# Kernel tuning notes

Hardware: AMD Instinct MI355X
Metric: run time of the kernel (lower is better)

The kernel has to match this reference:

```python
import math
import jax, jax.numpy as jnp
import numpy as np

B, T, D, K, R, KC = 4, 2048, 1024, 8, 16, 4
H = 4 * D  # mlp hidden


def setup_inputs() -> dict:
    key = jax.random.key(0)
    ks = jax.random.split(key, 12)
    s = lambda i, shape: jax.random.normal(ks[i], shape, jnp.float32) * 0.02
    # state_decay_logit init: geometric decays in [dmin, dmax], logit = log(p) - log1p(-p)
    dmin, dmax = 0.9, 0.999
    dec = np.exp(np.linspace(math.log(dmin), math.log(dmax), K))
    decay_logit = jnp.asarray(np.log(dec) - np.log1p(-dec), jnp.float32)
    return dict(
        x=jax.random.normal(ks[0], (B, T, D), jnp.float32),
        conv_w=s(1, (D, 1, KC)),            # depthwise conv kernel (torch Conv1d weight)
        gp_w=s(2, (D, D)), gp_b=jnp.zeros((D,), jnp.float32),
        up_w=s(3, (D, H)), up_b=jnp.zeros((H,), jnp.float32),
        dn_w=s(4, (H, D)), dn_b=jnp.zeros((D,), jnp.float32),
        si_w=s(5, (D, K * D)),              # state_in (no bias)
        so_w=s(6, (K * D, D)),              # state_out (no bias)
        decay_logit=decay_logit,
        rs_w=s(7, (D, R)), rs_b=jnp.zeros((R,), jnp.float32),
        rwg_w=s(8, (D, 1)), rwg_b=jnp.zeros((1,), jnp.float32),
        rv_w=s(9, (D, D)), rv_b=jnp.zeros((D,), jnp.float32),
        gr_w=s(10, (D, 1)), gr_b=jnp.zeros((1,), jnp.float32),
        gl_w=s(11, (D, 1)), gl_b=jnp.zeros((1,), jnp.float32),
    )


def _rms_norm(x, eps=1e-6):
    return x * jax.lax.rsqrt(jnp.mean(x * x, axis=-1, keepdims=True) + eps)


def _forward(x, conv_w, gp_w, gp_b, up_w, up_b, dn_w, dn_b, si_w, so_w,
             decay_logit, rs_w, rs_b, rwg_w, rwg_b, rv_w, rv_b, gr_w, gr_b, gl_w, gl_b):
    Bx, Tx, Dx = x.shape
    u = _rms_norm(x)
    # --- local mixer: causal depthwise conv + sigmoid gate + SiLU MLP ---
    xc = jax.lax.conv_general_dilated(
        jnp.swapaxes(u, 1, 2), conv_w, window_strides=(1,),
        padding=[(KC - 1, 0)], feature_group_count=Dx,
        dimension_numbers=('NCH', 'OIH', 'NCH'))
    xc = jnp.swapaxes(xc, 1, 2)                       # (B,T,D) causal conv output
    xg = xc * jax.nn.sigmoid(xc @ gp_w + gp_b)
    local = jax.nn.silu(xg @ up_w + up_b) @ dn_w + dn_b
    # --- per-channel exponential-decay state + register read/write scan ---
    dec = jax.nn.sigmoid(decay_logit)                 # (K,)
    z = (u @ si_w).reshape(Bx, Tx, K, Dx)             # state_in, (B,T,K,D)
    sel = jax.nn.softmax(u @ rs_w + rs_b, axis=-1)    # soft register address (B,T,R)
    wg = jax.nn.sigmoid(u @ rwg_w + rwg_b)            # write gate (B,T,1)
    v = u @ rv_w + rv_b                                # register value (B,T,D)

    def step(carry, inp):
        s, regs = carry
        z_t, sel_t, w_t, v_t = inp
        read = jnp.einsum('br,brd->bd', sel_t, regs)  # soft read before write
        ws = (w_t * sel_t)[:, :, None]                # (B,R,1)
        regs = regs * (1.0 - ws) + ws * v_t[:, None, :]
        s = dec[None, :, None] * s + z_t
        return (s, regs), (s, read)

    init = (jnp.zeros((Bx, K, Dx), x.dtype), jnp.zeros((Bx, R, Dx), x.dtype))
    tm = lambda a: jnp.swapaxes(a, 0, 1)              # time-major for scan
    _, (s_all, reads) = jax.lax.scan(step, init, (tm(z), tm(sel), tm(wg), tm(v)))
    s_all = tm(s_all)                                 # (B,T,K,D)
    reads = tm(reads)                                 # (B,T,D)
    long_out = jnp.einsum('btkd,kde->bte', s_all, so_w.reshape(K, Dx, Dx))
    g_long = jax.nn.sigmoid(u @ gl_w + gl_b)
    g_reg = jax.nn.sigmoid(u @ gr_w + gr_b)
    return x + local + g_long * long_out + g_reg * reads


def reference(x, conv_w, gp_w, gp_b, up_w, up_b, dn_w, dn_b, si_w, so_w,
              decay_logit, rs_w, rs_b, rwg_w, rwg_b, rv_w, rv_b, gr_w, gr_b, gl_w, gl_b):
    return _forward(x, conv_w, gp_w, gp_b, up_w, up_b, dn_w, dn_b, si_w, so_w,
                    decay_logit, rs_w, rs_b, rwg_w, rwg_b, rv_w, rv_b, gr_w, gr_b, gl_w, gl_b)
```

## Files before the change

kernel.cpp:

```cpp
#include <hip/hip_runtime.h>

typedef unsigned short u16;
typedef __bf16 bf16x8 __attribute__((ext_vector_type(8)));
typedef float f32x4 __attribute__((ext_vector_type(4)));
typedef u16 u16x4 __attribute__((ext_vector_type(4)));

#define D_ 1024
#define T_ 2048
#define B_ 4
#define K_ 8
#define R_ 16
#define H_ 4096
#define NROW (B_*T_)
#define CH 32
#define CL (T_/CH)
#define CHS 64
#define CLS (T_/CHS)

__device__ __forceinline__ u16 f2bf(float f){
  union{float f;unsigned u;} v; v.f=f;
  unsigned r = v.u + 0x7FFFu + ((v.u>>16)&1u);
  return (u16)(r>>16);
}
__device__ __forceinline__ float bf2f(u16 b){
  union{unsigned u;float f;} v; v.u = ((unsigned)b)<<16; return v.f;
}
__device__ __forceinline__ float sigm(float x){ return 1.f/(1.f+__expf(-x)); }

__device__ __forceinline__ void gload_lds16(const void* g, void* l){
  __builtin_amdgcn_global_load_lds((const __attribute__((address_space(1))) void*)g,
                                   (__attribute__((address_space(3))) void*)l, 16, 0, 0);
}

__global__ __launch_bounds__(256) void fill_k(float* __restrict__ out, long n, float v){
  long i = (long)blockIdx.x*256 + threadIdx.x;
  if (i < n) out[i] = v;
}

__global__ __launch_bounds__(256) void transpose_cast(const float* __restrict__ in, u16* __restrict__ out,
                                                      int R, int C){
  __shared__ float tile[32][33];
  int bx = blockIdx.x*32;
  int by = blockIdx.y*32;
  int tx = threadIdx.x & 31, ty = threadIdx.x >> 5;
  #pragma unroll
  for (int i=0;i<32;i+=8) tile[ty+i][tx] = in[(size_t)(by+ty+i)*C + bx+tx];
  __syncthreads();
  #pragma unroll
  for (int i=0;i<32;i+=8) out[(size_t)(bx+ty+i)*R + by+tx] = f2bf(tile[tx][ty+i]);
}

__global__ __launch_bounds__(256) void castbf(const float* __restrict__ in, u16* __restrict__ out, long n){
  long i = (long)blockIdx.x*256 + threadIdx.x;
  if (i < n) out[i] = f2bf(in[i]);
}

__global__ __launch_bounds__(256) void rmsnorm_fused(
    const float* __restrict__ x, const float* __restrict__ dn_b,
    const float* __restrict__ rs_w, const float* __restrict__ rs_b,
    const float* __restrict__ rwg_w, const float* __restrict__ rwg_b,
    const float* __restrict__ gl_w, const float* __restrict__ gl_b,
    const float* __restrict__ gr_w, const float* __restrict__ gr_b,
    u16* __restrict__ u, float* __restrict__ out,
    float* __restrict__ sel, float* __restrict__ wgb,
    float* __restrict__ glb, float* __restrict__ grb)
{
  int row = blockIdx.x, tid = threadIdx.x;
  const float* xr = x + (size_t)row*D_;
  float xv[4]; float ss = 0.f;
  #pragma unroll
  for (int i=0;i<4;i++){ xv[i] = xr[tid + 256*i]; ss += xv[i]*xv[i]; }
  #pragma unroll
  for (int o=32;o>0;o>>=1) ss += __shfl_down(ss, o);
  __shared__ float red0[4];
  if ((tid&63)==0) red0[tid>>6] = ss;
  __syncthreads();
  float tot = red0[0]+red0[1]+red0[2]+red0[3];
  float r = rsqrtf(tot*(1.f/D_) + 1e-6f);

  float p[19];
  #pragma unroll
  for (int c=0;c<19;c++) p[c] = 0.f;
  #pragma unroll
  for (int i=0;i<4;i++){
    int e = tid + 256*i;
    float ue = xv[i]*r;
    u[(size_t)row*D_ + e] = f2bf(ue);
    out[(size_t)row*D_ + e] = xv[i] + dn_b[e];
    const float* rw = rs_w + (size_t)e*16;
    #pragma unroll
    for (int c=0;c<16;c++) p[c] += ue*rw[c];
    p[16] += ue*rwg_w[e];
    p[17] += ue*gl_w[e];
    p[18] += ue*gr_w[e];
  }
  __shared__ float red[19*4];
  #pragma unroll
  for (int c=0;c<19;c++){
    float v = p[c];
    #pragma unroll
    for (int o=32;o>0;o>>=1) v += __shfl_down(v, o);
    if ((tid&63)==0) red[c*4 + (tid>>6)] = v;
  }
  __syncthreads();
  if (tid==0){
    float s[19];
    #pragma unroll
    for (int c=0;c<19;c++) s[c] = red[c*4]+red[c*4+1]+red[c*4+2]+red[c*4+3];
    float mx = -1e30f;
    #pragma unroll
    for (int c=0;c<16;c++){ s[c] += rs_b[c]; mx = fmaxf(mx, s[c]); }
    float ssum = 0.f;
    #pragma unroll
    for (int c=0;c<16;c++){ s[c] = __expf(s[c]-mx); ssum += s[c]; }
    float inv = 1.f/ssum;
    #pragma unroll
    for (int c=0;c<16;c++) sel[(size_t)row*16+c] = s[c]*inv;
    wgb[row] = sigm(s[16] + rwg_b[0]);
    glb[row] = sigm(s[17] + gl_b[0]);
    grb[row] = sigm(s[18] + gr_b[0]);
  }
}

__global__ __launch_bounds__(256) void rmsnorm_k(const float* __restrict__ x, u16* __restrict__ u){
  int row = blockIdx.x;
  const float* xr = x + (size_t)row*D_;
  float xv[4]; float ss = 0.f;
  #pragma unroll
  for (int i=0;i<4;i++){ xv[i] = xr[threadIdx.x + 256*i]; ss += xv[i]*xv[i]; }
  #pragma unroll
  for (int o=32;o>0;o>>=1) ss += __shfl_down(ss, o);
  __shared__ float red[4];
  if ((threadIdx.x&63)==0) red[threadIdx.x>>6] = ss;
  __syncthreads();
  float tot = red[0]+red[1]+red[2]+red[3];
  float r = rsqrtf(tot*(1.f/D_) + 1e-6f);
  #pragma unroll
  for (int i=0;i<4;i++) u[(size_t)row*D_ + threadIdx.x + 256*i] = f2bf(xv[i]*r);
}

__global__ __launch_bounds__(256) void conv_k(const u16* __restrict__ u, const float* __restrict__ w,
                                              u16* __restrict__ xc){
  size_t base = ((size_t)blockIdx.x*256 + threadIdx.x)*4;
  int t  = (int)((base >> 10) & (T_-1));
  int d0 = (int)(base & (D_-1));
  f32x4 wv[4];
  #pragma unroll
  for (int jj=0;jj<4;jj++) wv[jj] = *(const f32x4*)&w[(d0+jj)*4];
  float acc[4] = {0.f,0.f,0.f,0.f};
  #pragma unroll
  for (int j=0;j<4;j++){
    if (t-3+j >= 0){
      u16x4 uv = *(const u16x4*)(u + base + (long)(j-3)*D_);
      #pragma unroll
      for (int jj=0;jj<4;jj++) acc[jj] += bf2f(uv[jj]) * wv[jj][j];
    }
  }
  u16x4 o;
  #pragma unroll
  for (int jj=0;jj<4;jj++) o[jj] = f2bf(acc[jj]);
  *(u16x4*)(xc + base) = o;
}

__global__ __launch_bounds__(256) void smalln_k(const u16* __restrict__ u,
    const float* __restrict__ rs_w, const float* __restrict__ rs_b,
    const float* __restrict__ rwg_w, const float* __restrict__ rwg_b,
    const float* __restrict__ gl_w, const float* __restrict__ gl_b,
    const float* __restrict__ gr_w, const float* __restrict__ gr_b,
    float* __restrict__ sel, float* __restrict__ wg, float* __restrict__ gl, float* __restrict__ gr){
  int row = blockIdx.x, tid = threadIdx.x;
  float p[19];
  #pragma unroll
  for (int c=0;c<19;c++) p[c] = 0.f;
  for (int i=0;i<4;i++){
    int e = tid + i*256;
    float ue = bf2f(u[(size_t)row*D_ + e]);
    const float* rw = rs_w + (size_t)e*16;
    #pragma unroll
    for (int r=0;r<16;r++) p[r] += ue*rw[r];
    p[16] += ue*rwg_w[e];
    p[17] += ue*gl_w[e];
    p[18] += ue*gr_w[e];
  }
  __shared__ float red[19*4];
  #pragma unroll
  for (int c=0;c<19;c++){
    float v = p[c];
    #pragma unroll
    for (int o=32;o>0;o>>=1) v += __shfl_down(v, o);
    if ((tid&63)==0) red[c*4 + (tid>>6)] = v;
  }
  __syncthreads();
  if (tid==0){
    float s[19];
    #pragma unroll
    for (int c=0;c<19;c++) s[c] = red[c*4]+red[c*4+1]+red[c*4+2]+red[c*4+3];
    float mx = -1e30f;
    #pragma unroll
    for (int r=0;r<16;r++){ s[r] += rs_b[r]; mx = fmaxf(mx, s[r]); }
    float ssum = 0.f;
    #pragma unroll
    for (int r=0;r<16;r++){ s[r] = __expf(s[r]-mx); ssum += s[r]; }
    float inv = 1.f/ssum;
    #pragma unroll
    for (int r=0;r<16;r++) sel[(size_t)row*16+r] = s[r]*inv;
    wg[row] = sigm(s[16] + rwg_b[0]);
    gl[row] = sigm(s[17] + gl_b[0]);
    gr[row] = sigm(s[18] + gr_b[0]);
  }
}

#define BM 128
#define BN 128
#define BK 32

template<int EPI>
__global__ __launch_bounds__(256)
void gemm_bt(const u16* __restrict__ A, const u16* __restrict__ BT,
             void* __restrict__ outp, const float* __restrict__ bias,
             const void* __restrict__ aux,
             int K, int lda, int ldb, int ldc,
             long zA, long zB, long zC)
{
  __shared__ __attribute__((aligned(16))) u16 As[BM*BK];
  __shared__ __attribute__((aligned(16))) u16 Bs[BN*BK];
  int nwg = gridDim.x*gridDim.y;
  int bx = blockIdx.x, by = blockIdx.y;
  if ((nwg & 7) == 0){
    int bid = blockIdx.y*gridDim.x + blockIdx.x;
    int cpx = nwg >> 3;
    int s = (bid & 7)*cpx + (bid >> 3);
    bx = s % gridDim.x; by = s / gridDim.x;
  }
  const u16* Ab = A + (size_t)blockIdx.z*zA + (size_t)bx*BM*lda;
  const u16* Bb = BT + (size_t)blockIdx.z*zB + (size_t)by*BN*ldb;
  int tid = threadIdx.x, lane = tid&63, wid = tid>>6;
  int wr = wid>>1, wc = wid&1;
  f32x4 acc[4][4];
  #pragma unroll
  for (int m=0;m<4;m++)
    #pragma unroll
    for (int n=0;n<4;n++) acc[m][n] = (f32x4){0.f,0.f,0.f,0.f};

  int srow = lane>>2;
  int scol = (lane&3)*8;
  int klo  = (lane>>4)*8;
  for (int k0=0; k0<K; k0+=BK){
    #pragma unroll
    for (int i=0;i<2;i++){
      int r0 = wid*32 + i*16;
      gload_lds16(Ab + (size_t)(r0+srow)*lda + k0 + scol, &As[r0*BK]);
      gload_lds16(Bb + (size_t)(r0+srow)*ldb + k0 + scol, &Bs[r0*BK]);
    }
    __syncthreads();
    bf16x8 af[4], bfr[4];
    #pragma unroll
    for (int m=0;m<4;m++) af[m] = *(const bf16x8*)&As[(wr*64+m*16+(lane&15))*BK + klo];
    #pragma unroll
    for (int n=0;n<4;n++) bfr[n] = *(const bf16x8*)&Bs[(wc*64+n*16+(lane&15))*BK + klo];
    #pragma unroll
    for (int m=0;m<4;m++)
      #pragma unroll
      for (int n=0;n<4;n++)
        acc[m][n] = __builtin_amdgcn_mfma_f32_16x16x32_bf16(af[m], bfr[n], acc[m][n], 0, 0, 0);
    __syncthreads();
  }

  size_t obase = (size_t)blockIdx.z*zC;
  int row0 = bx*BM + wr*64;
  int col0 = by*BN + wc*64;
  #pragma unroll
  for (int m=0;m<4;m++){
    #pragma unroll
    for (int n=0;n<4;n++){
      int col = col0 + n*16 + (lane&15);
      #pragma unroll
      for (int r=0;r<4;r++){
        int row = row0 + m*16 + (lane>>4)*4 + r;
        float c = acc[m][n][r];
        size_t idx = obase + (size_t)row*ldc + col;
        if (EPI==0){ ((u16*)outp)[idx] = f2bf(c); }
        else if (EPI==1){ ((u16*)outp)[idx] = f2bf(c + bias[col]); }
        else if (EPI==2){ float t=c+bias[col]; ((u16*)outp)[idx] = f2bf(bf2f(((const u16*)aux)[idx]) * sigm(t)); }
        else if (EPI==3){ float t=c+bias[col]; ((u16*)outp)[idx] = f2bf(t*sigm(t)); }
        else if (EPI==4){ ((float*)outp)[idx] = ((const float*)aux)[idx] + c + bias[col]; }
        else            { ((float*)outp)[idx] += c; }
      }
    }
  }
}

template<int NT, int EPI>
__global__ __launch_bounds__(512, 2)
void gemm8p(const u16* __restrict__ A, const u16* __restrict__ BT,
            void* __restrict__ outp, const float* __restrict__ bias,
            const void* __restrict__ aux,
            int lda, int ldb, int ldc, long zA, long zB, long zC,
            int rx, int ry, int nry)
{
  __shared__ __attribute__((aligned(16))) u16 lds8[65536];
  int bid = blockIdx.y*gridDim.x + blockIdx.x;
  int xcd = bid & 7;
  int s   = bid >> 3;
  int rgx = xcd / nry, rgy = xcd - rgx*nry;
  int bx = rgx*rx + (s % rx);
  int by = rgy*ry + (s / rx);

  const u16* Ab = A + (size_t)blockIdx.z*zA + (size_t)bx*256*lda;
  const u16* Bb = BT + (size_t)blockIdx.z*zB + (size_t)by*256*ldb;

  int tid = threadIdx.x, l = tid&63, w = tid>>6;
  int wr = w>>2, wc = w&3;
  int rS0 = (w*2+0)*8 + (l>>3);
  int rS1 = (w*2+1)*8 + (l>>3);
  int cg  = (((l&7) ^ (l>>3)) << 3);
  int seg0 = (w*2+0)*512;
  int seg1 = (w*2+1)*512;

  auto STAGE = [&](int h){
    int kt = h>>2, idx = h&3, par = kt&1;
    int koff = kt*64;
    if (idx < 2){
      const u16* s0 = Bb + (size_t)(idx*128 + rS0)*ldb + koff + cg;
      const u16* s1 = Bb + (size_t)(idx*128 + rS1)*ldb + koff + cg;
      u16* d = &lds8[par*32768 + 16384 + idx*8192];
      gload_lds16(s0, d + seg0);
      gload_lds16(s1, d + seg1);
    } else {
      int a = idx-2;
      const u16* s0 = Ab + (size_t)(a*128 + rS0)*lda + koff + cg;
      const u16* s1 = Ab + (size_t)(a*128 + rS1)*lda + koff + cg;
      u16* d = &lds8[par*32768 + a*8192];
      gload_lds16(s0, d + seg0);
      gload_lds16(s1, d + seg1);
    }
  };

  f32x4 acc[8][4];
  #pragma unroll
  for (int m=0;m<8;m++)
    #pragma unroll
    for (int n=0;n<4;n++) acc[m][n] = (f32x4){0.f,0.f,0.f,0.f};

  for (int h=0; h<7; ++h) STAGE(h);
  asm volatile("s_waitcnt vmcnt(6)" ::: "memory");
  __builtin_amdgcn_s_barrier();

  for (int it=0; it<NT/2; ++it){
    #pragma unroll
    for (int sub=0; sub<2; ++sub){
      int kt = it*2+sub;
      const int par = sub;
      u16* Abase = &lds8[par*32768 + wr*8192];
      u16* Bbase = &lds8[par*32768 + 16384 + (wc>>1)*8192];
      bf16x8 bf[4][2];
      #pragma unroll
      for (int q=0; q<4; ++q){
        bf16x8 af[2][2];
        if (q==0){
          #pragma unroll
          for (int n=0;n<4;n++)
            #pragma unroll
            for (int ss=0;ss<2;ss++){
              int rr = (wc&1)*64 + n*16 + (l&15);
              int c16 = (l>>4) + ss*4;
              bf[n][ss] = *(const bf16x8*)&Bbase[rr*64 + ((c16 ^ (rr&7))<<3)];
            }
        }
        #pragma unroll
        for (int i=0;i<2;i++)
          #pragma unroll
          for (int ss=0;ss<2;ss++){
            int rr = q*32 + i*16 + (l&15);
            int c16 = (l>>4) + ss*4;
            af[i][ss] = *(const bf16x8*)&Abase[rr*64 + ((c16 ^ (rr&7))<<3)];
          }
        __builtin_amdgcn_sched_barrier(0);
        int h = kt*4 + q + 7;
        if (h < 4*NT) STAGE(h);
        __builtin_amdgcn_s_barrier();
        asm volatile("s_waitcnt lgkmcnt(0)" ::: "memory");
        __builtin_amdgcn_sched_barrier(0);
        __builtin_amdgcn_s_setprio(1);
        #pragma unroll
        for (int i=0;i<2;i++)
          #pragma unroll
          for (int n=0;n<4;n++)
            #pragma unroll
            for (int ss=0;ss<2;ss++)
              acc[q*2+i][n] = __builtin_amdgcn_mfma_f32_16x16x32_bf16(af[i][ss], bf[n][ss], acc[q*2+i][n], 0, 0, 0);
        __builtin_amdgcn_s_setprio(0);
        if (q==3){
          if (kt == NT-2)      asm volatile("s_waitcnt vmcnt(0)" ::: "memory");
          else if (kt < NT-2)  asm volatile("s_waitcnt vmcnt(6)" ::: "memory");
        }
        __builtin_amdgcn_s_barrier();
      }
    }
  }

  size_t obase = (size_t)blockIdx.z*zC;
  int row0 = bx*256 + wr*128;
  int col0 = by*256 + wc*64;
  #pragma unroll
  for (int m=0;m<8;m++){
    #pragma unroll
    for (int n=0;n<4;n++){
      int col = col0 + n*16 + (l&15);
      #pragma unroll
      for (int r=0;r<4;r++){
        int row = row0 + m*16 + (l>>4)*4 + r;
        float c = acc[m][n][r];
        size_t idx = obase + (size_t)row*ldc + col;
        if (EPI==0){ ((u16*)outp)[idx] = f2bf(c); }
        else if (EPI==1){ ((u16*)outp)[idx] = f2bf(c + bias[col]); }
        else if (EPI==2){ float t=c+bias[col]; ((u16*)outp)[idx] = f2bf(bf2f(((const u16*)aux)[idx]) * sigm(t)); }
        else if (EPI==3){ float t=c+bias[col]; ((u16*)outp)[idx] = f2bf(t*sigm(t)); }
        else            { unsafeAtomicAdd(&((float*)outp)[idx], c); }
      }
    }
  }
}

template<int NT>
__global__ __launch_bounds__(512, 2)
void gemm8z(const u16* __restrict__ A, const u16* __restrict__ BT,
            void* __restrict__ outp, const float* __restrict__ bias,
            const float* __restrict__ bias2, const void* __restrict__ aux,
            int lda, int ldb, int ldc, long zA, long zB, long zC,
            int rx, int ry, int nry)
{
  __shared__ __attribute__((aligned(16))) u16 lds8[65536];
  int bid = blockIdx.y*gridDim.x + blockIdx.x;
  int xcd = bid & 7;
  int s   = bid >> 3;
  int rgx = xcd / nry, rgy = xcd - rgx*nry;
  int bx = rgx*rx + (s % rx);
  int by = rgy*ry + (s / rx);

  const u16* Ab = A + (size_t)blockIdx.z*zA + (size_t)bx*256*lda;
  const u16* Bb = BT + (size_t)blockIdx.z*zB + (size_t)by*256*ldb;

  int tid = threadIdx.x, l = tid&63, w = tid>>6;
  int wr = w>>2, wc = w&3;
  int rS0 = (w*2+0)*8 + (l>>3);
  int rS1 = (w*2+1)*8 + (l>>3);
  int cg  = (((l&7) ^ (l>>3)) << 3);
  int seg0 = (w*2+0)*512;
  int seg1 = (w*2+1)*512;

  auto STAGE = [&](int h){
    int kt = h>>2, idx = h&3, par = kt&1;
    int koff = kt*64;
    if (idx < 2){
      const u16* s0 = Bb + (size_t)(idx*128 + rS0)*ldb + koff + cg;
      const u16* s1 = Bb + (size_t)(idx*128 + rS1)*ldb + koff + cg;
      u16* d = &lds8[par*32768 + 16384 + idx*8192];
      gload_lds16(s0, d + seg0);
      gload_lds16(s1, d + seg1);
    } else {
      int a = idx-2;
      const u16* s0 = Ab + (size_t)(a*128 + rS0)*lda + koff + cg;
      const u16* s1 = Ab + (size_t)(a*128 + rS1)*lda + koff + cg;
      u16* d = &lds8[par*32768 + a*8192];
      gload_lds16(s0, d + seg0);
      gload_lds16(s1, d + seg1);
    }
  };

  f32x4 acc[8][4];
  #pragma unroll
  for (int m=0;m<8;m++)
    #pragma unroll
    for (int n=0;n<4;n++) acc[m][n] = (f32x4){0.f,0.f,0.f,0.f};

  for (int h=0; h<7; ++h) STAGE(h);
  asm volatile("s_waitcnt vmcnt(6)" ::: "memory");
  __builtin_amdgcn_s_barrier();

  for (int it=0; it<NT/2; ++it){
    #pragma unroll
    for (int sub=0; sub<2; ++sub){
      int kt = it*2+sub;
      const int par = sub;
      u16* Abase = &lds8[par*32768 + wr*8192];
      u16* Bbase = &lds8[par*32768 + 16384 + (wc>>1)*8192];
      bf16x8 bf[4][2];
      #pragma unroll
      for (int q=0; q<4; ++q){
        bf16x8 af[2][2];
        if (q==0){
          #pragma unroll
          for (int n=0;n<4;n++)
            #pragma unroll
            for (int ss=0;ss<2;ss++){
              int rr = (wc&1)*64 + n*16 + (l&15);
              int c16 = (l>>4) + ss*4;
              bf[n][ss] = *(const bf16x8*)&Bbase[rr*64 + ((c16 ^ (rr&7))<<3)];
            }
        }
        #pragma unroll
        for (int i=0;i<2;i++)
          #pragma unroll
          for (int ss=0;ss<2;ss++){
            int rr = q*32 + i*16 + (l&15);
            int c16 = (l>>4) + ss*4;
            af[i][ss] = *(const bf16x8*)&Abase[rr*64 + ((c16 ^ (rr&7))<<3)];
          }
        __builtin_amdgcn_sched_barrier(0);
        int h = kt*4 + q + 7;
        if (h < 4*NT) STAGE(h);
        __builtin_amdgcn_s_barrier();
        asm volatile("s_waitcnt lgkmcnt(0)" ::: "memory");
        __builtin_amdgcn_sched_barrier(0);
        __builtin_amdgcn_s_setprio(1);
        #pragma unroll
        for (int i=0;i<2;i++)
          #pragma unroll
          for (int n=0;n<4;n++)
            #pragma unroll
            for (int ss=0;ss<2;ss++)
              acc[q*2+i][n] = __builtin_amdgcn_mfma_f32_16x16x32_bf16(af[i][ss], bf[n][ss], acc[q*2+i][n], 0, 0, 0);
        __builtin_amdgcn_s_setprio(0);
        if (q==3){
          if (kt == NT-2)      asm volatile("s_waitcnt vmcnt(0)" ::: "memory");
          else if (kt < NT-2)  asm volatile("s_waitcnt vmcnt(6)" ::: "memory");
        }
        __builtin_amdgcn_s_barrier();
      }
    }
  }

  size_t obase = (size_t)blockIdx.z*zC;
  int row0 = bx*256 + wr*128;
  int col0 = by*256 + wc*64;
  bool z0 = (blockIdx.z == 0);
  #pragma unroll
  for (int m=0;m<8;m++){
    #pragma unroll
    for (int n=0;n<4;n++){
      int col = col0 + n*16 + (l&15);
      #pragma unroll
      for (int r=0;r<4;r++){
        int row = row0 + m*16 + (l>>4)*4 + r;
        float c = acc[m][n][r];
        size_t idx = obase + (size_t)row*ldc + col;
        if (z0){ float t=c+bias[col]; ((u16*)outp)[idx] = f2bf(bf2f(((const u16*)aux)[idx]) * sigm(t)); }
        else   { ((u16*)outp)[idx] = f2bf(c + bias2[col]); }
      }
    }
  }
}

template<int KH>
__global__ __launch_bounds__(256) void scan_s1k(const u16* __restrict__ y, const float* __restrict__ logit,
                                                int p, float* __restrict__ Hend){
  int k = blockIdx.x;
  int e0 = threadIdx.x*4;
  int c = blockIdx.y, b = blockIdx.z;
  float dec = sigm(logit[KH*p+k]);
  f32x4 h = (f32x4){0.f,0.f,0.f,0.f};
  size_t row0 = (size_t)b*T_ + (size_t)c*CLS;
  for (int t=0;t<CLS;t++){
    u16x4 w = *(const u16x4*)(y + (row0+t)*(size_t)(KH*D_) + (size_t)k*D_ + e0);
    #pragma unroll
    for (int j=0;j<4;j++) h[j] = dec*h[j] + bf2f(w[j]);
  }
  *(f32x4*)&Hend[(((size_t)b*CHS+c)*KH+k)*D_ + e0] = h;
}

template<int KH>
__global__ __launch_bounds__(256) void scan_s2v(const float* __restrict__ Hend, const float* __restrict__ logit,
                                                int p, float* __restrict__ Sinit){
  int idx = blockIdx.x*256 + threadIdx.x;
  if (idx >= B_*KH*D_) return;
  int e = idx % D_; int kh = (idx/D_) % KH; int b = idx/(D_*KH);
  float dec = sigm(logit[KH*p+kh]);
  float dL = powf(dec, (float)CLS);
  float carry = 0.f;
  for (int c=0;c<CHS;c++){
    size_t i3 = (((size_t)b*CHS+c)*KH+kh)*D_ + e;
    Sinit[i3] = carry;
    carry = dL*carry + Hend[i3];
  }
}

template<int KH>
__global__ __launch_bounds__(128) void scan_s3v(const u16* __restrict__ y, const float* __restrict__ logit,
                                                int p, const float* __restrict__ Sinit,
                                                const float* __restrict__ glb, float* __restrict__ out){
  int e0 = (blockIdx.x*128 + threadIdx.x)*4;
  int c = blockIdx.y, b = blockIdx.z;
  float dec[KH]; f32x4 h[KH];
  #pragma unroll
  for (int k=0;k<KH;k++){
    dec[k] = sigm(logit[KH*p+k]);
    h[k] = *(const f32x4*)&Sinit[(((size_t)b*CHS+c)*KH+k)*D_ + e0];
  }
  size_t row0 = (size_t)b*T_ + (size_t)c*CLS;
  for (int t=0;t<CLS;t++){
    const u16* yp = y + (row0+t)*(size_t)(KH*D_) + e0;
    f32x4 sum = (f32x4){0.f,0.f,0.f,0.f};
    #pragma unroll
    for (int k=0;k<KH;k++){
      u16x4 w = *(const u16x4*)(yp + (size_t)k*D_);
      #pragma unroll
      for (int j=0;j<4;j++){ h[k][j] = dec[k]*h[k][j] + bf2f(w[j]); sum[j] += h[k][j]; }
    }
    float g = glb[row0+t];
    f32x4* op = (f32x4*)&out[(row0+t)*D_ + e0];
    f32x4 ov = *op;
    #pragma unroll
    for (int j=0;j<4;j++) ov[j] += g*sum[j];
    *op = ov;
  }
}

__global__ __launch_bounds__(128) void scan_s3r(
    const u16* __restrict__ y, const float* __restrict__ logit, int p,
    const float* __restrict__ Sinit,
    const u16* __restrict__ v, const float* __restrict__ sel,
    const float* __restrict__ wg, const float* __restrict__ Rinit,
    const float* __restrict__ glb, const float* __restrict__ grb,
    float* __restrict__ out)
{
  int d = blockIdx.x*128 + threadIdx.x;
  int c = blockIdx.y, b = blockIdx.z;
  __shared__ float sel_s[64*R_];
  __shared__ float wg_s[64], gl_s[64], gr_s[64];
  size_t row0 = (size_t)b*T_ + (size_t)c*64;
  for (int i=threadIdx.x; i<64*R_; i+=128) sel_s[i] = sel[row0*R_ + i];
  for (int i=threadIdx.x; i<64; i+=128){
    wg_s[i] = wg[row0+i]; gl_s[i] = glb[row0+i]; gr_s[i] = grb[row0+i];
  }
  __syncthreads();
  float dec[4], h[4];
  #pragma unroll
  for (int k=0;k<4;k++){
    dec[k] = sigm(logit[4*p+k]);
    h[k] = Sinit[(((size_t)b*CHS + 2*c)*4 + k)*D_ + d];
  }
  float regs[R_];
  #pragma unroll
  for (int r=0;r<R_;r++) regs[r] = Rinit[(((size_t)b*CH+c)*R_+r)*D_ + d];
  for (int t=0;t<64;t++){
    const u16* yp = y + (row0+t)*(size_t)(4*D_) + d;
    float sum = 0.f;
    #pragma unroll
    for (int k=0;k<4;k++){ h[k] = dec[k]*h[k] + bf2f(yp[(size_t)k*D_]); sum += h[k]; }
    float vv = bf2f(v[(row0+t)*D_ + d]);
    float w = wg_s[t];
    float read = 0.f;
    #pragma unroll
    for (int r=0;r<R_;r++){
      float sr = sel_s[t*R_+r];
      read += sr*regs[r];
      float ws = w*sr;
      regs[r] += ws*(vv - regs[r]);
    }
    out[(row0+t)*D_ + d] += gl_s[t]*sum + gr_s[t]*read;
  }
}

__global__ __launch_bounds__(256) void scan_r1(const u16* __restrict__ v, const float* __restrict__ sel,
                                               const float* __restrict__ wg,
                                               float* __restrict__ Rend, float* __restrict__ Pout){
  int d = blockIdx.x*256 + threadIdx.x;
  int c = blockIdx.y, b = blockIdx.z;
  __shared__ float sel_s[CL*R_];
  __shared__ float wg_s[CL];
  size_t row0 = (size_t)b*T_ + (size_t)c*CL;
  for (int i=threadIdx.x; i<CL*R_; i+=256) sel_s[i] = sel[row0*R_ + i];
  for (int i=threadIdx.x; i<CL;    i+=256) wg_s[i]  = wg[row0 + i];
  __syncthreads();
  float regs[R_], P[R_];
  #pragma unroll
  for (int r=0;r<R_;r++){ regs[r]=0.f; P[r]=1.f; }
  for (int t=0;t<CL;t++){
    float vv = bf2f(v[(row0+t)*D_ + d]);
    float w = wg_s[t];
    #pragma unroll
    for (int r=0;r<R_;r++){
      float ws = w*sel_s[t*R_+r];
      regs[r] += ws*(vv - regs[r]);
      P[r] *= (1.f - ws);
    }
  }
  #pragma unroll
  for (int r=0;r<R_;r++) Rend[(((size_t)b*CH+c)*R_+r)*D_ + d] = regs[r];
  if (blockIdx.x==0 && threadIdx.x==0){
    #pragma unroll
    for (int r=0;r<R_;r++) Pout[((size_t)b*CH+c)*R_ + r] = P[r];
  }
}

__global__ __launch_bounds__(256) void scan_r2(const float* __restrict__ Rend, const float* __restrict__ Pbuf,
                                               float* __restrict__ Rinit){
  int idx = blockIdx.x*256 + threadIdx.x;
  if (idx >= B_*D_) return;
  int d = idx % D_; int b = idx / D_;
  float regs[R_];
  #pragma unroll
  for (int r=0;r<R_;r++) regs[r] = 0.f;
  for (int c=0;c<CH;c++){
    #pragma unroll
    for (int r=0;r<R_;r++){
      size_t i3 = (((size_t)b*CH+c)*R_+r)*D_ + d;
      Rinit[i3] = regs[r];
      regs[r] = Pbuf[((size_t)b*CH+c)*R_+r]*regs[r] + Rend[i3];
    }
  }
}

__global__ __launch_bounds__(256) void scan_r3(const u16* __restrict__ v, const float* __restrict__ sel,
                                               const float* __restrict__ wg, const float* __restrict__ Rinit,
                                               const float* __restrict__ grb, float* __restrict__ out){
  int d = blockIdx.x*256 + threadIdx.x;
  int c = blockIdx.y, b = blockIdx.z;
  __shared__ float sel_s[CL*R_];
  __shared__ float wg_s[CL];
  size_t row0 = (size_t)b*T_ + (size_t)c*CL;
  for (int i=threadIdx.x; i<CL*R_; i+=256) sel_s[i] = sel[row0*R_ + i];
  for (int i=threadIdx.x; i<CL;    i+=256) wg_s[i]  = wg[row0 + i];
  __syncthreads();
  float regs[R_];
  #pragma unroll
  for (int r=0;r<R_;r++) regs[r] = Rinit[(((size_t)b*CH+c)*R_+r)*D_ + d];
  for (int t=0;t<CL;t++){
    float vv = bf2f(v[(row0+t)*D_ + d]);
    float w = wg_s[t];
    float read = 0.f;
    #pragma unroll
    for (int r=0;r<R_;r++){
      float sr = sel_s[t*R_+r];
      read += sr*regs[r];
      float ws = w*sr;
      regs[r] += ws*(vv - regs[r]);
    }
    out[(row0+t)*D_ + d] += grb[row0+t]*read;
  }
}

static void launch_gemm(int epi, dim3 g, const u16* A, const u16* BT, void* out,
                        const float* bias, const void* aux, int K, int lda, int ldb, int ldc,
                        long zA, long zB, long zC, hipStream_t s){
  switch(epi){
    case 0: gemm_bt<0><<<g,256,0,s>>>(A,BT,out,bias,aux,K,lda,ldb,ldc,zA,zB,zC); break;
    case 1: gemm_bt<1><<<g,256,0,s>>>(A,BT,out,bias,aux,K,lda,ldb,ldc,zA,zB,zC); break;
    case 2: gemm_bt<2><<<g,256,0,s>>>(A,BT,out,bias,aux,K,lda,ldb,ldc,zA,zB,zC); break;
    case 3: gemm_bt<3><<<g,256,0,s>>>(A,BT,out,bias,aux,K,lda,ldb,ldc,zA,zB,zC); break;
    case 4: gemm_bt<4><<<g,256,0,s>>>(A,BT,out,bias,aux,K,lda,ldb,ldc,zA,zB,zC); break;
    default: gemm_bt<5><<<g,256,0,s>>>(A,BT,out,bias,aux,K,lda,ldb,ldc,zA,zB,zC); break;
  }
}

extern "C" void kernel_launch(void* const* d_in, const int* in_sizes, int n_in,
                              void* d_out, int out_size, void* d_ws, size_t ws_size,
                              hipStream_t stream){
  const float* x      = (const float*)d_in[0];
  const float* conv_w = (const float*)d_in[1];
  const float* gp_w   = (const float*)d_in[2];
  const float* gp_b   = (const float*)d_in[3];
  const float* up_w   = (const float*)d_in[4];
  const float* up_b   = (const float*)d_in[5];
  const float* dn_w   = (const float*)d_in[6];
  const float* dn_b   = (const float*)d_in[7];
  const float* si_w   = (const float*)d_in[8];
  const float* so_w   = (const float*)d_in[9];
  const float* logit  = (const float*)d_in[10];
  const float* rs_w   = (const float*)d_in[11];
  const float* rs_b   = (const float*)d_in[12];
  const float* rwg_w  = (const float*)d_in[13];
  const float* rwg_b  = (const float*)d_in[14];
  const float* rv_w   = (const float*)d_in[15];
  const float* rv_b   = (const float*)d_in[16];
  const float* gr_w   = (const float*)d_in[17];
  const float* gr_b   = (const float*)d_in[18];
  const float* gl_w   = (const float*)d_in[19];
  const float* gl_b   = (const float*)d_in[20];
  float* out = (float*)d_out;
  char* base = (char*)d_ws;

  {
    size_t off = 0;
    auto al = [&](size_t b)->char*{ char* r = base+off; off += (b+255)&~(size_t)255; return r; };
    char* u_r    = al((size_t)NROW*D_*2);
    char* v_r    = al((size_t)NROW*D_*2);
    char* big    = al((size_t)121634816);
    float* sel   = (float*)al((size_t)NROW*R_*4);
    float* wgb   = (float*)al((size_t)NROW*4);
    float* glb   = (float*)al((size_t)NROW*4);
    float* grb   = (float*)al((size_t)NROW*4);
    float* Pbuf  = (float*)al((size_t)B_*CH*R_*4);
    float* Rend  = (float*)al((size_t)B_*CH*R_*D_*4);
    float* Rinit = (float*)al((size_t)B_*CH*R_*D_*4);
    if (off <= ws_size){
      u16* u_bf  = (u16*)u_r;
      u16* v_bf  = (u16*)v_r;
      u16* hid   = (u16*)big;
      u16* xc_bf = (u16*)(big + (size_t)67108864);
      u16* xg_bf = (u16*)(big + (size_t)83886080);
      u16* gpT   = (u16*)(big + (size_t)100663296);
      u16* upT   = (u16*)(big + (size_t)102760448);
      u16* dnT   = (u16*)(big + (size_t)111149056);
      u16* rvT   = (u16*)(big + (size_t)119537664);
      u16* WT    = (u16*)big;
      u16* si_bf = (u16*)(big + (size_t)16777216);
      u16* soT   = (u16*)(big + (size_t)33554432);
      u16* y_bf  = (u16*)(big + (size_t)16777216);
      float* Hend  = (float*)(big + (size_t)83886080);
      float* Sinit = (float*)(big + (size_t)88080384);

      transpose_cast<<<dim3(D_/32, D_/32),256,0,stream>>>(gp_w, gpT, D_, D_);
      transpose_cast<<<dim3(H_/32, D_/32),256,0,stream>>>(up_w, upT, D_, H_);
      transpose_cast<<<dim3(D_/32, H_/32),256,0,stream>>>(dn_w, dnT, H_, D_);
      transpose_cast<<<dim3(D_/32, D_/32),256,0,stream>>>(rv_w, rvT, D_, D_);

      rmsnorm_fused<<<NROW,256,0,stream>>>(x, dn_b, rs_w, rs_b, rwg_w, rwg_b,
                                           gl_w, gl_b, gr_w, gr_b,
                                           u_bf, out, sel, wgb, glb, grb);
      conv_k<<<(NROW*D_)/1024,256,0,stream>>>(u_bf, conv_w, xc_bf);

      gemm8z<16><<<dim3(NROW/256, D_/256, 2), 512, 0, stream>>>(
          xc_bf, gpT, xg_bf, gp_b, rv_b, xc_bf, D_, D_, D_,
          (long)(u_bf - xc_bf), (long)(rvT - gpT), (long)(v_bf - xg_bf), 4, 4, 1);

      gemm8p<16,3><<<dim3(NROW/256, H_/256), 512, 0, stream>>>(
          xg_bf, upT, hid, up_b, nullptr, D_, D_, H_, 0, 0, 0, 8, 8, 2);

      gemm8p<32,5><<<dim3(NROW/256, D_/256, 2), 512, 0, stream>>>(
          hid, dnT, out, nullptr, nullptr, H_, H_, D_, 2048, 2048, 0, 4, 4, 1);

      transpose_cast<<<dim3(D_/32, (K_*D_)/32),256,0,stream>>>(so_w, soT, K_*D_, D_);
      castbf<<<((long)D_*K_*D_+255)/256,256,0,stream>>>(si_w, si_bf, (long)D_*K_*D_);
      launch_gemm(0, dim3(D_/BM, D_/BN, K_), soT, si_bf, WT, nullptr, nullptr,
                  D_, K_*D_, K_*D_, D_, (long)D_, (long)D_, (long)D_*D_, stream);

      scan_r1<<<dim3(D_/256, CH, B_),256,0,stream>>>(v_bf, sel, wgb, Rend, Pbuf);
      scan_r2<<<(B_*D_+255)/256,256,0,stream>>>(Rend, Pbuf, Rinit);

      gemm8p<16,0><<<dim3(NROW/256, (4*D_)/256), 512, 0, stream>>>(
          u_bf, WT, y_bf, nullptr, nullptr, D_, D_, 4*D_, 0, 0, 0, 8, 8, 2);
      scan_s1k<4><<<dim3(4, CHS, B_),256,0,stream>>>(y_bf, logit, 0, Hend);
      scan_s2v<4><<<(B_*4*D_+255)/256,256,0,stream>>>(Hend, logit, 0, Sinit);
      scan_s3v<4><<<dim3(2, CHS, B_),128,0,stream>>>(y_bf, logit, 0, Sinit, glb, out);

      gemm8p<16,0><<<dim3(NROW/256, (4*D_)/256), 512, 0, stream>>>(
          u_bf, WT + (size_t)4*D_*D_, y_bf, nullptr, nullptr, D_, D_, 4*D_, 0, 0, 0, 8, 8, 2);
      scan_s1k<4><<<dim3(4, CHS, B_),256,0,stream>>>(y_bf, logit, 1, Hend);
      scan_s2v<4><<<(B_*4*D_+255)/256,256,0,stream>>>(Hend, logit, 1, Sinit);
      scan_s3r<<<dim3(D_/128, CH, B_),128,0,stream>>>(
          y_bf, logit, 1, Sinit, v_bf, sel, wgb, Rinit, glb, grb, out);
      return;
    }
  }

  const size_t MB16_8 = (size_t)NROW*D_*2;
  size_t off = 0;
  auto alloc = [&](size_t bytes)->char*{
    char* r = base + off; off += (bytes + 255) & ~(size_t)255; return r;
  };
  char* R0 = alloc(MB16_8);
  char* R1 = alloc(MB16_8);
  char* R2 = alloc(2*MB16_8);
  char* R3 = alloc((size_t)21*1024*1024);
  float* sel  = (float*)alloc((size_t)NROW*R_*4);
  float* wgb  = (float*)alloc((size_t)NROW*4);
  float* glb  = (float*)alloc((size_t)NROW*4);
  float* grb  = (float*)alloc((size_t)NROW*4);
  float* Pbuf = (float*)alloc((size_t)B_*CH*R_*4);
  float* Hend = (float*)alloc((size_t)B_*CHS*2*D_*4);
  float* Sinit= (float*)alloc((size_t)B_*CHS*2*D_*4);
  if (off > ws_size){
    fill_k<<<((long)out_size+255)/256,256,0,stream>>>(out, out_size, 12345.0f);
    return;
  }

  u16* u_bf  = (u16*)R0;
  u16* v_bf  = (u16*)R1;
  u16* xc_bf = (u16*)R2;
  u16* xg_bf = (u16*)(R2 + MB16_8);
  u16* hid_bf= (u16*)R2;
  u16* soT   = (u16*)R2;
  u16* si_bf = (u16*)(R2 + MB16_8);
  u16* y_bf  = (u16*)R2;
  u16* gpT   = (u16*)R3;
  u16* upT   = (u16*)(R3 + (size_t)2*1024*1024 + 131072);
  u16* dnT   = (u16*)(R3 + (size_t)10*1024*1024 + 655360);
  u16* rvT   = (u16*)(R3 + (size_t)19*1024*1024);
  u16* WT    = (u16*)R3;
  float* Rend = (float*)R3;
  float* Rinit= (float*)(R3 + (size_t)NROW*D_);

  transpose_cast<<<dim3(D_/32, D_/32),256,0,stream>>>(gp_w, gpT, D_, D_);
  transpose_cast<<<dim3(H_/32, D_/32),256,0,stream>>>(up_w, upT, D_, H_);
  transpose_cast<<<dim3(D_/32, H_/32),256,0,stream>>>(dn_w, dnT, H_, D_);
  transpose_cast<<<dim3(D_/32, D_/32),256,0,stream>>>(rv_w, rvT, D_, D_);

  rmsnorm_k<<<NROW,256,0,stream>>>(x, u_bf);
  conv_k<<<(NROW*D_)/1024,256,0,stream>>>(u_bf, conv_w, xc_bf);
  smalln_k<<<NROW,256,0,stream>>>(u_bf, rs_w, rs_b, rwg_w, rwg_b, gl_w, gl_b, gr_w, gr_b,
                                  sel, wgb, glb, grb);

  launch_gemm(2, dim3(NROW/BM, D_/BN, 1), xc_bf, gpT, xg_bf, gp_b, xc_bf,
              D_, D_, D_, D_, 0, 0, 0, stream);
  launch_gemm(1, dim3(NROW/BM, D_/BN, 1), u_bf, rvT, v_bf, rv_b, nullptr,
              D_, D_, D_, D_, 0, 0, 0, stream);
  for (int q=0; q<4; q++){
    launch_gemm(3, dim3(NROW/BM, 1024/BN, 1), xg_bf, upT + (size_t)q*1024*D_, hid_bf,
                up_b + q*1024, nullptr, D_, D_, D_, 1024, 0, 0, 0, stream);
    launch_gemm(q==0?4:5, dim3(NROW/BM, D_/BN, 1), hid_bf, dnT + (size_t)q*1024, out,
                dn_b, x, 1024, 1024, H_, D_, 0, 0, 0, stream);
  }

  transpose_cast<<<dim3(D_/32, (K_*D_)/32),256,0,stream>>>(so_w, soT, K_*D_, D_);
  castbf<<<((long)D_*K_*D_+255)/256,256,0,stream>>>(si_w, si_bf, (long)D_*K_*D_);
  launch_gemm(0, dim3(D_/BM, D_/BN, K_), soT, si_bf, WT, nullptr, nullptr,
              D_, K_*D_, K_*D_, D_, (long)D_, (long)D_, (long)D_*D_, stream);

  for (int p=0; p<4; p++){
    launch_gemm(0, dim3(NROW/BM, (2*D_)/BN, 1), u_bf, WT + (size_t)(2*p)*D_*D_, y_bf,
                nullptr, nullptr, D_, D_, D_, 2*D_, 0, 0, 0, stream);
    scan_s1k<2><<<dim3(2, CHS, B_),256,0,stream>>>(y_bf, logit, p, Hend);
    scan_s2v<2><<<(B_*2*D_+255)/256,256,0,stream>>>(Hend, logit, p, Sinit);
    scan_s3v<2><<<dim3(2, CHS, B_),128,0,stream>>>(y_bf, logit, p, Sinit, glb, out);
  }

  scan_r1<<<dim3(D_/256, CH, B_),256,0,stream>>>(v_bf, sel, wgb, Rend, Pbuf);
  scan_r2<<<(B_*D_+255)/256,256,0,stream>>>(Rend, Pbuf, Rinit);
  scan_r3<<<dim3(D_/256, CH, B_),256,0,stream>>>(v_bf, sel, wgb, Rinit, grb, out);
}
```

Baseline: 712.0 us.

## Add half-size LDS double-buffered GEMM variant for first state projection

```diff
diff --git a/kernel.cpp b/kernel.cpp
--- a/kernel.cpp
+++ b/kernel.cpp
@@ -552,6 +552,115 @@
   }
 }
 
+template<int NT, int EPI>
+__global__ __launch_bounds__(512, 4)
+void gemm8h(const u16* __restrict__ A, const u16* __restrict__ BT,
+            void* __restrict__ outp, const float* __restrict__ bias,
+            const void* __restrict__ aux,
+            int lda, int ldb, int ldc, long zA, long zB, long zC,
+            int rx, int ry, int nry)
+{
+  __shared__ __attribute__((aligned(16))) u16 ldsh[32768];
+  int bid = blockIdx.y*gridDim.x + blockIdx.x;
+  int xcd = bid & 7;
+  int s   = bid >> 3;
+  int rgx = xcd / nry, rgy = xcd - rgx*nry;
+  int bx = rgx*rx + (s % rx);
+  int by = rgy*ry + (s / rx);
+
+  const u16* Ab = A + (size_t)blockIdx.z*zA + (size_t)bx*256*lda;
+  const u16* Bb = BT + (size_t)blockIdx.z*zB + (size_t)by*256*ldb;
+
+  int tid = threadIdx.x, l = tid&63, w = tid>>6;
+  int wr = w>>2, wc = w&3;
+  int rS = tid>>2;
+  int cgh = (((tid&3) ^ ((rS>>1)&3)) << 3);
+
+  auto STAGEH = [&](int h){
+    int kt = h>>2, idx = h&3, par = kt&1;
+    int koff = kt*32;
+    if (idx < 2){
+      gload_lds16(Bb + (size_t)(idx*128 + rS)*ldb + koff + cgh,
+                  &ldsh[par*16384 + 8192 + idx*4096 + tid*8]);
+    } else {
+      int a = idx-2;
+      gload_lds16(Ab + (size_t)(a*128 + rS)*lda + koff + cgh,
+                  &ldsh[par*16384 + a*4096 + tid*8]);
+    }
+  };
+
+  f32x4 acc[8][4];
+  #pragma unroll
+  for (int m=0;m<8;m++)
+    #pragma unroll
+    for (int n=0;n<4;n++) acc[m][n] = (f32x4){0.f,0.f,0.f,0.f};
+
+  for (int h=0; h<7; ++h) STAGEH(h);
+  asm volatile("s_waitcnt vmcnt(3)" ::: "memory");
+  __builtin_amdgcn_s_barrier();
+
+  int sl = l>>4;
+  for (int kt=0; kt<NT; ++kt){
+    const int par = kt&1;
+    const u16* Ah = &ldsh[par*16384];
+    const u16* Bh = &ldsh[par*16384 + 8192];
+    bf16x8 bf[4];
+    #pragma unroll
+    for (int q=0; q<4; ++q){
+      bf16x8 af[2];
+      if (q==0){
+        #pragma unroll
+        for (int n=0;n<4;n++){
+          int rr = wc*64 + n*16 + (l&15);
+          bf[n] = *(const bf16x8*)&Bh[(rr>>7)*4096 + (rr&127)*32 + ((sl ^ ((rr>>1)&3))<<3)];
+        }
+      }
+      #pragma unroll
+      for (int i=0;i<2;i++){
+        int rr = wr*128 + (q*2+i)*16 + (l&15);
+        af[i] = *(const bf16x8*)&Ah[(rr>>7)*4096 + (rr&127)*32 + ((sl ^ ((rr>>1)&3))<<3)];
+      }
+      int h = kt*4 + q + 7;
+      if (h < 4*NT) STAGEH(h);
+      __builtin_amdgcn_s_barrier();
+      asm volatile("s_waitcnt lgkmcnt(0)" ::: "memory");
+      __builtin_amdgcn_s_setprio(1);
+      #pragma unroll
+      for (int i=0;i<2;i++)
+        #pragma unroll
+        for (int n=0;n<4;n++)
+          acc[q*2+i][n] = __builtin_amdgcn_mfma_f32_16x16x32_bf16(af[i], bf[n], acc[q*2+i][n], 0, 0, 0);
+      __builtin_amdgcn_s_setprio(0);
+      if (q==3){
+        if (kt == NT-2)      asm volatile("s_waitcnt vmcnt(0)" ::: "memory");
+        else if (kt < NT-2)  asm volatile("s_waitcnt vmcnt(3)" ::: "memory");
+      }
+      __builtin_amdgcn_s_barrier();
+    }
+  }
+
+  size_t obase = (size_t)blockIdx.z*zC;
+  int row0 = bx*256 + wr*128;
+  int col0 = by*256 + wc*64;
+  #pragma unroll
+  for (int m=0;m<8;m++){
+    #pragma unroll
+    for (int n=0;n<4;n++){
+      int col = col0 + n*16 + (l&15);
+      #pragma unroll
+      for (int r=0;r<4;r++){
+        int row = row0 + m*16 + (l>>4)*4 + r;
+        float c = acc[m][n][r];
+        size_t idx = obase + (size_t)row*ldc + col;
+        if (EPI==0){ ((u16*)outp)[idx] = f2bf(c); }
+        else if (EPI==1){ ((u16*)outp)[idx] = f2bf(c + bias[col]); }
+        else if (EPI==3){ float t=c+bias[col]; ((u16*)outp)[idx] = f2bf(t*sigm(t)); }
+        else            { unsafeAtomicAdd(&((float*)outp)[idx], c); }
+      }
+    }
+  }
+}
+
 template<int KH>
 __global__ __launch_bounds__(256) void scan_s1k(const u16* __restrict__ y, const float* __restrict__ logit,
                                                 int p, float* __restrict__ Hend){
@@ -839,7 +948,7 @@
       scan_r1<<<dim3(D_/256, CH, B_),256,0,stream>>>(v_bf, sel, wgb, Rend, Pbuf);
       scan_r2<<<(B_*D_+255)/256,256,0,stream>>>(Rend, Pbuf, Rinit);
 
-      gemm8p<16,0><<<dim3(NROW/256, (4*D_)/256), 512, 0, stream>>>(
+      gemm8h<32,0><<<dim3(NROW/256, (4*D_)/256), 512, 0, stream>>>(
           u_bf, WT, y_bf, nullptr, nullptr, D_, D_, 4*D_, 0, 0, 0, 8, 8, 2);
       scan_s1k<4><<<dim3(4, CHS, B_),256,0,stream>>>(y_bf, logit, 0, Hend);
       scan_s2v<4><<<(B_*4*D_+255)/256,256,0,stream>>>(Hend, logit, 0, Sinit);
```

Measured after the change: 1.215 ms. +70.7%, slower.
